# Optimization experiments

Measured on AMD Instinct MI355X. Metric: run time of the kernel, lower is better.

The kernel has to match this reference:

```python
import jax, jax.numpy as jnp
import numpy as np

B, L, D = 8, 4096, 256
G, K = 64, 8          # n_groups, group_size
N = G * K             # 512 slots
H = 8                 # attention heads
EPS = 1e-5

def _ln(x, g, b):
    m = jnp.mean(x, axis=-1, keepdims=True)
    v = jnp.var(x, axis=-1, keepdims=True)
    return (x - m) * jax.lax.rsqrt(v + EPS) * g + b

def _gelu(x):
    return jax.nn.gelu(x, approximate=False)  # torch nn.GELU default = exact erf

def setup_inputs() -> dict:
    key = jax.random.key(0)
    ks = jax.random.split(key, 24)
    s = 0.02
    d = {
        'X': jax.random.normal(ks[0], (B, L, D), jnp.float32),
        'S': jax.random.normal(ks[1], (B, N, D), jnp.float32),
        'Wg':  jax.random.normal(ks[2], (D, G)) * s,
        'Wk':  jax.random.normal(ks[3], (D, K)) * s,
        'Wm1': jax.random.normal(ks[4], (D, 2*D)) * s, 'bm1': jnp.zeros((2*D,)),
        'Wm2': jax.random.normal(ks[5], (2*D, D)) * s, 'bm2': jnp.zeros((D,)),
        'Wgt1': jax.random.normal(ks[6], (D, D)) * s, 'bgt1': jnp.zeros((D,)),
        'Wgt2': jax.random.normal(ks[7], (D, 1)) * s, 'bgt2': jnp.zeros((1,)),
        'Wqkv': jax.random.normal(ks[8], (D, 3*D)) * s, 'bqkv': jnp.zeros((3*D,)),
        'Wo':  jax.random.normal(ks[9], (D, D)) * s, 'bo': jnp.zeros((D,)),
        'aln_g': jnp.ones((D,)), 'aln_b': jnp.zeros((D,)),
        'Wu1': jax.random.normal(ks[10], (2*D, 2*D)) * s, 'bu1': jnp.zeros((2*D,)),
        'Wu2': jax.random.normal(ks[11], (2*D, D)) * s, 'bu2': jnp.zeros((D,)),
        'ln_g': jnp.ones((D,)), 'ln_b': jnp.zeros((D,)),
    }
    return d

def reference(X, S, Wg, Wk, Wm1, bm1, Wm2, bm2, Wgt1, bgt1, Wgt2, bgt2,
              Wqkv, bqkv, Wo, bo, aln_g, aln_b, Wu1, bu1, Wu2, bu2, ln_g, ln_b):
    # --- hierarchical routing (eval path: argmax one-hot) ---
    msg = _gelu(X @ Wm1 + bm1) @ Wm2 + bm2                 # (B,L,D)
    gate = jax.nn.sigmoid(_gelu(X @ Wgt1 + bgt1) @ Wgt2 + bgt2)  # (B,L,1)
    gm = msg * gate
    gidx = jnp.argmax(X @ Wg, axis=-1)                     # (B,L)
    kidx = jnp.argmax(X @ Wk, axis=-1)                     # (B,L)
    idx = gidx * K + kidx                                  # flat slot id in [0,N)
    full = jax.nn.one_hot(idx, N, dtype=X.dtype)           # (B,L,N)
    incoming = jnp.einsum('bln,bld->bnd', full, gm)        # (B,N,D)
    # --- slot self-attention ---
    qkv = S @ Wqkv + bqkv
    q, k, v = jnp.split(qkv, 3, axis=-1)
    dh = D // H
    q = q.reshape(B, N, H, dh); k = k.reshape(B, N, H, dh); v = v.reshape(B, N, H, dh)
    scores = jnp.einsum('bqhd,bkhd->bhqk', q, k) / jnp.sqrt(jnp.asarray(dh, X.dtype))
    attn = jax.nn.softmax(scores, axis=-1)
    o = jnp.einsum('bhqk,bkhd->bqhd', attn, v).reshape(B, N, D) @ Wo + bo
    S1 = _ln(S + o, aln_g, aln_b)
    # --- update ---
    cat = jnp.concatenate([S1, incoming], axis=-1)         # (B,N,2D)
    S2 = S1 + _gelu(cat @ Wu1 + bu1) @ Wu2 + bu2
    return _ln(S2, ln_g, ln_b)
```

## Files before the change

kernel.cpp:

```cpp
#include <hip/hip_runtime.h>

typedef __bf16 bf16_t;
typedef __bf16 bf16x8 __attribute__((ext_vector_type(8)));
typedef __bf16 bf16x4v __attribute__((ext_vector_type(4)));
typedef __bf16 bf16x2v __attribute__((ext_vector_type(2)));
typedef float f32x4 __attribute__((ext_vector_type(4)));
typedef unsigned long long u64;

#define LN_EPS 1e-5f

__device__ __forceinline__ float erf_fast(float a) {
  const float t = fabsf(a);
  const float s = a * a;
  float r;
  if (t > 0.921875f) {
    float u;
    r = fmaf(-1.72853470e-5f, t, 3.83197126e-4f);
    u = fmaf(-3.88396438e-3f, t, 2.42546219e-2f);
    r = fmaf(r, s, u);
    r = fmaf(r, t, 1.06777877e-1f);
    r = fmaf(r, t, -6.37245935e-1f);
    r = fmaf(r, t, -1.28717512e-1f);
    r = fmaf(r, t, t);
    r = 1.0f - __expf(-r);
    r = copysignf(r, a);
  } else {
    r = -5.96761703e-4f;
    r = fmaf(r, s, 4.99119423e-3f);
    r = fmaf(r, s, -2.67681349e-2f);
    r = fmaf(r, s, 1.12819925e-1f);
    r = fmaf(r, s, -3.76125336e-1f);
    r = fmaf(r, s, 1.28379166e-1f);
    r = fmaf(r, a, a);
  }
  return r;
}

__device__ __forceinline__ float gelu_f(float x) {
  const float h = 0.5f * x;
  return fmaf(h, erf_fast(x * 0.70710678118654752f), h);
}

__device__ __forceinline__ void async16(const bf16_t* g, bf16_t* l) {
  __builtin_amdgcn_global_load_lds(
      (const __attribute__((address_space(1))) void*)g,
      (__attribute__((address_space(3))) void*)l, 16, 0, 0);
}

__global__ __launch_bounds__(256)
void prep_kernel(const float* __restrict__ X, const float* __restrict__ S,
                 const float* __restrict__ Wg, const float* __restrict__ Wk,
                 const float* __restrict__ Wm1, const float* __restrict__ Wgt1,
                 const float* __restrict__ Wm2, const float* __restrict__ Wqkv,
                 const float* __restrict__ Wo, const float* __restrict__ Wu1,
                 const float* __restrict__ Wu2,
                 bf16_t* __restrict__ Xb, bf16_t* __restrict__ Sb,
                 bf16_t* __restrict__ W1t, bf16_t* __restrict__ W2t,
                 bf16_t* __restrict__ Wqkvt, bf16_t* __restrict__ Wot,
                 bf16_t* __restrict__ Wu1t, bf16_t* __restrict__ Wu2t,
                 float4* __restrict__ zbase)
{
  const int bid = blockIdx.x;
  const int t = threadIdx.x;
  if (bid < 8192) {
    const int i = bid * 256 + t;
    const float4 v = ((const float4*)X)[i];
    bf16x4v o; o[0]=(bf16_t)v.x; o[1]=(bf16_t)v.y; o[2]=(bf16_t)v.z; o[3]=(bf16_t)v.w;
    ((bf16x4v*)Xb)[i] = o;
  } else if (bid < 9216) {
    const int i = (bid - 8192) * 256 + t;
    const float4 v = ((const float4*)S)[i];
    bf16x4v o; o[0]=(bf16_t)v.x; o[1]=(bf16_t)v.y; o[2]=(bf16_t)v.z; o[3]=(bf16_t)v.w;
    ((bf16x4v*)Sb)[i] = o;
  } else if (bid < 10112) {
    const int n = bid - 9216;
    const int k = t;
    float v;
    if (n < 512)      v = Wm1[k * 512 + n];
    else if (n < 768) v = Wgt1[k * 256 + (n - 512)];
    else if (n < 832) v = Wg[k * 64 + (n - 768)];
    else if (n < 840) v = Wk[k * 8 + (n - 832)];
    else              v = 0.f;
    W1t[n * 256 + k] = (bf16_t)v;
  } else if (bid < 10368) {
    const int n = bid - 10112;
    for (int k = t; k < 512; k += 256) W2t[n * 512 + k] = (bf16_t)Wm2[k * 256 + n];
  } else if (bid < 11136) {
    const int n = bid - 10368;
    Wqkvt[n * 256 + t] = (bf16_t)Wqkv[t * 768 + n];
  } else if (bid < 11392) {
    const int n = bid - 11136;
    Wot[n * 256 + t] = (bf16_t)Wo[t * 256 + n];
  } else if (bid < 11904) {
    const int n = bid - 11392;
    for (int k = t; k < 512; k += 256) Wu1t[n * 512 + k] = (bf16_t)Wu1[k * 512 + n];
  } else if (bid < 12160) {
    const int n = bid - 11904;
    for (int k = t; k < 512; k += 256) Wu2t[n * 512 + k] = (bf16_t)Wu2[k * 256 + n];
  } else {
    zbase[(bid - 12160) * 256 + t] = make_float4(0.f, 0.f, 0.f, 0.f);
  }
}

__global__ __launch_bounds__(256, 2)
void g1_kernel(const bf16_t* __restrict__ A,
               const bf16_t* __restrict__ Bt,
               const float* __restrict__ bias, const float* __restrict__ bias2,
               bf16_t* __restrict__ h1,
               const float* __restrict__ wgt2, float* __restrict__ gatelin,
               u64* __restrict__ bitmap)
{
  const int m0 = blockIdx.x * 128;
  const int by = blockIdx.y;
  const int n0 = by * 128;
  const int t = threadIdx.x;
  const int w = t >> 6;
  const int lane = t & 63;
  const int wr = w >> 1, wc = w & 1;
  const int quad = lane >> 4, l15 = lane & 15;

  __shared__ bf16_t lA[128 * 32];
  __shared__ bf16_t lB[128 * 32];
  __shared__ float sWg[256];
  __shared__ int sKi[128];

  if (by >= 4 && by < 6) sWg[t] = wgt2[t];

  f32x4 acc[4][4];
#pragma unroll
  for (int mt = 0; mt < 4; ++mt)
#pragma unroll
    for (int nt = 0; nt < 4; ++nt)
      acc[mt][nt] = (f32x4){0.f, 0.f, 0.f, 0.f};

  const int srow = t >> 2;
  const int schunk = ((t & 3) ^ (srow & 3)) * 8;
  const int ko = ((quad ^ (l15 & 3)) << 3);

  for (int k0 = 0; k0 < 256; k0 += 32) {
#pragma unroll
    for (int i = 0; i < 2; ++i) {
      const int row = i * 64 + srow;
      async16(A + (size_t)(m0 + row) * 256 + k0 + schunk,
              lA + (size_t)(i * 256 + (t & 192)) * 8);
      async16(Bt + (size_t)(n0 + row) * 256 + k0 + schunk,
              lB + (size_t)(i * 256 + (t & 192)) * 8);
    }
    __syncthreads();
    bf16x8 af[4], bfr[4];
#pragma unroll
    for (int mt = 0; mt < 4; ++mt)
      af[mt] = *(const bf16x8*)&lA[(wr * 64 + mt * 16 + l15) * 32 + ko];
#pragma unroll
    for (int nt = 0; nt < 4; ++nt)
      bfr[nt] = *(const bf16x8*)&lB[(wc * 64 + nt * 16 + l15) * 32 + ko];
#pragma unroll
    for (int mt = 0; mt < 4; ++mt)
#pragma unroll
      for (int nt = 0; nt < 4; ++nt)
        acc[mt][nt] = __builtin_amdgcn_mfma_f32_16x16x32_bf16(bfr[nt], af[mt], acc[mt][nt], 0, 0, 0);
    __syncthreads();
  }

  if (by < 4) {
#pragma unroll
    for (int mt = 0; mt < 4; ++mt) {
      const int row = m0 + wr * 64 + mt * 16 + l15;
#pragma unroll
      for (int nt = 0; nt < 4; ++nt) {
        const int colb = n0 + wc * 64 + nt * 16 + quad * 4;
        const float4 bb = *(const float4*)&bias[colb];
        bf16x4v o;
        o[0] = (bf16_t)gelu_f(acc[mt][nt][0] + bb.x);
        o[1] = (bf16_t)gelu_f(acc[mt][nt][1] + bb.y);
        o[2] = (bf16_t)gelu_f(acc[mt][nt][2] + bb.z);
        o[3] = (bf16_t)gelu_f(acc[mt][nt][3] + bb.w);
        *(bf16x4v*)&h1[(size_t)row * 512 + colb] = o;
      }
    }
  } else if (by < 6) {
#pragma unroll
    for (int mt = 0; mt < 4; ++mt) {
      const int row = m0 + wr * 64 + mt * 16 + l15;
      float part = 0.f;
#pragma unroll
      for (int nt = 0; nt < 4; ++nt) {
        const int colb = n0 + wc * 64 + nt * 16 + quad * 4;
        const int c = colb - 512;
        const float4 bb = *(const float4*)&bias2[c];
        part = fmaf(gelu_f(acc[mt][nt][0] + bb.x), sWg[c + 0], part);
        part = fmaf(gelu_f(acc[mt][nt][1] + bb.y), sWg[c + 1], part);
        part = fmaf(gelu_f(acc[mt][nt][2] + bb.z), sWg[c + 2], part);
        part = fmaf(gelu_f(acc[mt][nt][3] + bb.w), sWg[c + 3], part);
      }
      part += __shfl_xor(part, 16, 64);
      part += __shfl_xor(part, 32, 64);
      if (lane < 16) atomicAdd(&gatelin[row], part);
    }
  } else {
    int bi[4];
#pragma unroll
    for (int mt = 0; mt < 4; ++mt) {
      if (wc == 0) {
        float mv = -1e30f; int mi = 0;
#pragma unroll
        for (int nt = 0; nt < 4; ++nt)
#pragma unroll
          for (int j = 0; j < 4; ++j) {
            const int gc = nt * 16 + quad * 4 + j;
            const float v = acc[mt][nt][j];
            if (v > mv || (v == mv && gc < mi)) { mv = v; mi = gc; }
          }
#pragma unroll
        for (int off = 16; off <= 32; off <<= 1) {
          const float ov = __shfl_xor(mv, off, 64);
          const int oi = __shfl_xor(mi, off, 64);
          if (ov > mv || (ov == mv && oi < mi)) { mv = ov; mi = oi; }
        }
        bi[mt] = mi;
      } else {
        float mv = -1e30f; int mi = 0;
        if (quad < 2) {
#pragma unroll
          for (int j = 0; j < 4; ++j) {
            const int kc = quad * 4 + j;
            const float v = acc[mt][0][j];
            if (v > mv || (v == mv && kc < mi)) { mv = v; mi = kc; }
          }
        }
#pragma unroll
        for (int off = 16; off <= 32; off <<= 1) {
          const float ov = __shfl_xor(mv, off, 64);
          const int oi = __shfl_xor(mi, off, 64);
          if (ov > mv || (ov == mv && oi < mi)) { mv = ov; mi = oi; }
        }
        if (lane < 16) sKi[wr * 64 + mt * 16 + l15] = mi;
      }
    }
    __syncthreads();
    if (wc == 0 && lane < 16) {
#pragma unroll
      for (int mt = 0; mt < 4; ++mt) {
        const int rl = wr * 64 + mt * 16 + l15;
        const int row = m0 + rl;
        const int idx = bi[mt] * 8 + sKi[rl];
        const int b = row >> 12, tok = row & 4095;
        atomicOr(&bitmap[(size_t)(b * 512 + idx) * 64 + (tok >> 6)],
                 1ull << (tok & 63));
      }
    }
  }
}

template<int MT, int EPI>
__global__ __launch_bounds__(256)
void gemm_kernel(const bf16_t* __restrict__ A, int lda,
                 const bf16_t* __restrict__ Bt, int K,
                 const float* __restrict__ bias, const float* __restrict__ bias2,
                 void* __restrict__ outp, int ldc,
                 const float* __restrict__ wgt2, float* __restrict__ gatelin,
                 u64* __restrict__ bitmap)
{
  constexpr int BM = MT * 32;
  constexpr int CA = BM * 4;
  const int m0 = blockIdx.x * BM;
  const int by = blockIdx.y;
  const int n0 = by * 128;
  const int t = threadIdx.x;
  const int w = t >> 6;
  const int lane = t & 63;
  const int wr = w >> 1, wc = w & 1;
  const int quad = lane >> 4, l15 = lane & 15;

  __shared__ bf16_t lA[BM * 32];
  __shared__ bf16_t lB[128 * 32];

  f32x4 acc[MT][4];
#pragma unroll
  for (int mt = 0; mt < MT; ++mt)
#pragma unroll
    for (int nt = 0; nt < 4; ++nt)
      acc[mt][nt] = (f32x4){0.f, 0.f, 0.f, 0.f};

  for (int k0 = 0; k0 < K; k0 += 32) {
    if constexpr (CA >= 256) {
#pragma unroll
      for (int i = 0; i < CA / 256; ++i) {
        const int c = i * 256 + t;
        async16(A + (size_t)(m0 + (c >> 2)) * lda + k0 + (c & 3) * 8,
                lA + (size_t)(i * 256 + (t & 192)) * 8);
      }
    } else {
      if (t < CA)
        async16(A + (size_t)(m0 + (t >> 2)) * lda + k0 + (t & 3) * 8,
                lA + (size_t)(t & 192) * 8);
    }
#pragma unroll
    for (int i = 0; i < 2; ++i) {
      const int c = i * 256 + t;
      async16(Bt + (size_t)(n0 + (c >> 2)) * K + k0 + (c & 3) * 8,
              lB + (size_t)(i * 256 + (t & 192)) * 8);
    }
    __syncthreads();
    bf16x8 af[MT], bfr[4];
    const int ko = quad * 8;
#pragma unroll
    for (int mt = 0; mt < MT; ++mt)
      af[mt] = *(const bf16x8*)&lA[(wr * MT * 16 + mt * 16 + l15) * 32 + ko];
#pragma unroll
    for (int nt = 0; nt < 4; ++nt)
      bfr[nt] = *(const bf16x8*)&lB[(wc * 64 + nt * 16 + l15) * 32 + ko];
#pragma unroll
    for (int mt = 0; mt < MT; ++mt)
#pragma unroll
      for (int nt = 0; nt < 4; ++nt)
        acc[mt][nt] = __builtin_amdgcn_mfma_f32_16x16x32_bf16(bfr[nt], af[mt], acc[mt][nt], 0, 0, 0);
    __syncthreads();
  }

#pragma unroll
  for (int mt = 0; mt < MT; ++mt) {
    const int row = m0 + wr * MT * 16 + mt * 16 + l15;
#pragma unroll
    for (int nt = 0; nt < 4; ++nt) {
      const int colb = n0 + wc * 64 + nt * 16 + quad * 4;
      const float4 bb = *(const float4*)&bias[colb];
      bf16x4v o;
      o[0]=(bf16_t)gelu_f(acc[mt][nt][0]+bb.x); o[1]=(bf16_t)gelu_f(acc[mt][nt][1]+bb.y);
      o[2]=(bf16_t)gelu_f(acc[mt][nt][2]+bb.z); o[3]=(bf16_t)gelu_f(acc[mt][nt][3]+bb.w);
      *(bf16x4v*)&((bf16_t*)outp)[(size_t)row * ldc + colb] = o;
    }
  }
  (void)bias2; (void)wgt2; (void)gatelin; (void)bitmap;
}

__global__ __launch_bounds__(256)
void pair64_kernel(const bf16_t* __restrict__ H, const bf16_t* __restrict__ W2t,
                   const float* __restrict__ bm2, const float* __restrict__ sumg,
                   float* __restrict__ incom,
                   const bf16_t* __restrict__ Sb, const bf16_t* __restrict__ Wqkvt,
                   const float* __restrict__ bqkv, bf16_t* __restrict__ qkvb,
                   bf16_t* __restrict__ Vt)
{
  int id = blockIdx.x;
  const bool first = id < 128;
  if (!first) id -= 128;
  const bf16_t* A  = first ? H : Sb;
  const bf16_t* Bt = first ? W2t : Wqkvt;
  const float* bias = first ? bm2 : bqkv;
  const int lda = first ? 512 : 256;
  const int K   = first ? 512 : 256;
  const int m0 = (id & 63) * 64;
  const int n0 = (id >> 6) * 128;
  const int t = threadIdx.x;
  const int w = t >> 6;
  const int lane = t & 63;
  const int wr = w >> 1, wc = w & 1;
  const int quad = lane >> 4, l15 = lane & 15;

  __shared__ bf16_t lA[64 * 32];
  __shared__ bf16_t lB[128 * 32];

  f32x4 acc[2][4];
#pragma unroll
  for (int mt = 0; mt < 2; ++mt)
#pragma unroll
    for (int nt = 0; nt < 4; ++nt)
      acc[mt][nt] = (f32x4){0.f, 0.f, 0.f, 0.f};

  for (int k0 = 0; k0 < K; k0 += 32) {
    async16(A + (size_t)(m0 + (t >> 2)) * lda + k0 + (t & 3) * 8,
            lA + (size_t)(t & 192) * 8);
#pragma unroll
    for (int i = 0; i < 2; ++i) {
      const int c = i * 256 + t;
      async16(Bt + (size_t)(n0 + (c >> 2)) * K + k0 + (c & 3) * 8,
              lB + (size_t)(i * 256 + (t & 192)) * 8);
    }
    __syncthreads();
    bf16x8 af[2], bfr[4];
    const int ko = quad * 8;
#pragma unroll
    for (int mt = 0; mt < 2; ++mt)
      af[mt] = *(const bf16x8*)&lA[(wr * 32 + mt * 16 + l15) * 32 + ko];
#pragma unroll
    for (int nt = 0; nt < 4; ++nt)
      bfr[nt] = *(const bf16x8*)&lB[(wc * 64 + nt * 16 + l15) * 32 + ko];
#pragma unroll
    for (int mt = 0; mt < 2; ++mt)
#pragma unroll
      for (int nt = 0; nt < 4; ++nt)
        acc[mt][nt] = __builtin_amdgcn_mfma_f32_16x16x32_bf16(bfr[nt], af[mt], acc[mt][nt], 0, 0, 0);
    __syncthreads();
  }

  if (first) {
#pragma unroll
    for (int mt = 0; mt < 2; ++mt) {
      const int row = m0 + wr * 32 + mt * 16 + l15;
      const float gt = sumg[row];
#pragma unroll
      for (int nt = 0; nt < 4; ++nt) {
        const int colb = n0 + wc * 64 + nt * 16 + quad * 4;
        const float4 bb = *(const float4*)&bias[colb];
        *(float4*)&incom[(size_t)row * 256 + colb] =
            make_float4(fmaf(gt, bb.x, acc[mt][nt][0]), fmaf(gt, bb.y, acc[mt][nt][1]),
                        fmaf(gt, bb.z, acc[mt][nt][2]), fmaf(gt, bb.w, acc[mt][nt][3]));
      }
    }
  } else if (n0 < 512) {
#pragma unroll
    for (int mt = 0; mt < 2; ++mt) {
      const int row = m0 + wr * 32 + mt * 16 + l15;
#pragma unroll
      for (int nt = 0; nt < 4; ++nt) {
        const int colb = n0 + wc * 64 + nt * 16 + quad * 4;
        const float4 bb = *(const float4*)&bias[colb];
        bf16x4v o; o[0]=(bf16_t)(acc[mt][nt][0]+bb.x); o[1]=(bf16_t)(acc[mt][nt][1]+bb.y);
        o[2]=(bf16_t)(acc[mt][nt][2]+bb.z); o[3]=(bf16_t)(acc[mt][nt][3]+bb.w);
        *(bf16x4v*)&qkvb[(size_t)row * 768 + colb] = o;
      }
    }
  } else {
#pragma unroll
    for (int mt = 0; mt < 2; ++mt) {
      const int row = m0 + wr * 32 + mt * 16 + l15;
      const int b = row >> 9, key = row & 511;
#pragma unroll
      for (int nt = 0; nt < 4; ++nt) {
        const int colb = n0 + wc * 64 + nt * 16 + quad * 4;
        const int c = colb - 512;
        const int h2 = c >> 5, dh = c & 31;
        const float4 bb = *(const float4*)&bias[colb];
        bf16_t* vb = Vt + ((size_t)(b * 8 + h2) * 32 + dh) * 512 + key;
        vb[0]   = (bf16_t)(acc[mt][nt][0] + bb.x);
        vb[512] = (bf16_t)(acc[mt][nt][1] + bb.y);
        vb[1024]= (bf16_t)(acc[mt][nt][2] + bb.z);
        vb[1536]= (bf16_t)(acc[mt][nt][3] + bb.w);
      }
    }
  }
}

__global__ __launch_bounds__(256)
void gather_kernel(const bf16_t* __restrict__ h1, const float* __restrict__ gatelin,
                   const float* __restrict__ bgt2, const u64* __restrict__ bitmap,
                   bf16_t* __restrict__ H, float* __restrict__ sumg)
{
  const int bs = blockIdx.x;
  const int b = bs >> 9;
  const int t = threadIdx.x;
  __shared__ u64 sw[64];
  if (t < 64) sw[t] = bitmap[(size_t)bs * 64 + t];
  __syncthreads();
  const float bg = bgt2[0];
  float a0 = 0.f, a1 = 0.f, sg = 0.f;
  for (int wd = 0; wd < 64; ++wd) {
    u64 word = sw[wd];
    while (word) {
      const int bit = __builtin_ctzll(word);
      word &= word - 1;
      const int l = (b << 12) + (wd << 6) + bit;
      const float g = 1.0f / (1.0f + __expf(-(gatelin[l] + bg)));
      const bf16x2v hv = *(const bf16x2v*)&h1[(size_t)l * 512 + t * 2];
      a0 = fmaf(g, (float)hv[0], a0);
      a1 = fmaf(g, (float)hv[1], a1);
      sg += g;
    }
  }
  bf16x2v o; o[0] = (bf16_t)a0; o[1] = (bf16_t)a1;
  *(bf16x2v*)&H[(size_t)bs * 512 + t * 2] = o;
  if (t == 0) sumg[bs] = sg;
}

__global__ __launch_bounds__(256)
void attn_kernel(const bf16_t* __restrict__ qkv, const bf16_t* __restrict__ Vt,
                 bf16_t* __restrict__ obuf)
{
  const int bid = blockIdx.x;
  const int qc = bid & 15;
  const int h = (bid >> 4) & 7;
  const int b = bid >> 7;
  const int t = threadIdx.x;
  const int w = t >> 6, lane = t & 63;
  const int quad = lane >> 4, l15 = lane & 15;

  __shared__ bf16_t sP[32 * 520];
  __shared__ float sL[32];

  bf16x8 qf[2];
#pragma unroll
  for (int mt = 0; mt < 2; ++mt) {
    const int row = b * 512 + qc * 32 + mt * 16 + l15;
    qf[mt] = *(const bf16x8*)&qkv[(size_t)row * 768 + h * 32 + quad * 8];
  }
  const float scale = 0.17677669529663687f;
  for (int kt = w; kt < 32; kt += 4) {
    const int key = b * 512 + kt * 16 + l15;
    const bf16x8 kf = *(const bf16x8*)&qkv[(size_t)key * 768 + 256 + h * 32 + quad * 8];
#pragma unroll
    for (int mt = 0; mt < 2; ++mt) {
      f32x4 c = (f32x4){0.f, 0.f, 0.f, 0.f};
      c = __builtin_amdgcn_mfma_f32_16x16x32_bf16(qf[mt], kf, c, 0, 0, 0);
#pragma unroll
      for (int r = 0; r < 4; ++r)
        sP[(mt * 16 + quad * 4 + r) * 520 + kt * 16 + l15] = (bf16_t)(c[r] * scale);
    }
  }
  __syncthreads();

#pragma unroll
  for (int ri = 0; ri < 8; ++ri) {
    const int row = w * 8 + ri;
    const bf16x8 sv = *(const bf16x8*)&sP[row * 520 + lane * 8];
    float sval[8];
    float mx = -1e30f;
#pragma unroll
    for (int j = 0; j < 8; ++j) { sval[j] = (float)sv[j]; mx = fmaxf(mx, sval[j]); }
#pragma unroll
    for (int off = 32; off; off >>= 1) mx = fmaxf(mx, __shfl_xor(mx, off, 64));
    float sum = 0.f;
    bf16x8 pv;
#pragma unroll
    for (int j = 0; j < 8; ++j) { const float e = __expf(sval[j] - mx); sum += e; pv[j] = (bf16_t)e; }
#pragma unroll
    for (int off = 32; off; off >>= 1) sum += __shfl_xor(sum, off, 64);
    *(bf16x8*)&sP[row * 520 + lane * 8] = pv;
    if (lane == 0) sL[row] = sum;
  }
  __syncthreads();

  const int wq = w >> 1, wd = w & 1;
  const bf16_t* vbase = Vt + ((size_t)(b * 8 + h) * 32 + wd * 16 + l15) * 512;
  const bf16_t* pbase = &sP[(wq * 16 + l15) * 520];
  f32x4 oacc = (f32x4){0.f, 0.f, 0.f, 0.f};
#pragma unroll
  for (int kt = 0; kt < 16; ++kt) {
    const bf16x8 af = *(const bf16x8*)&pbase[kt * 32 + quad * 8];
    const bf16x8 vf = *(const bf16x8*)&vbase[kt * 32 + quad * 8];
    oacc = __builtin_amdgcn_mfma_f32_16x16x32_bf16(vf, af, oacc, 0, 0, 0);
  }
  const int rowq = wq * 16 + l15;
  const float inv = 1.0f / sL[rowq];
  bf16x4v o;
#pragma unroll
  for (int r = 0; r < 4; ++r) o[r] = (bf16_t)(oacc[r] * inv);
  *(bf16x4v*)&obuf[(size_t)(b * 512 + qc * 32 + rowq) * 256 + h * 32 + wd * 16 + quad * 4] = o;
}

__global__ __launch_bounds__(256)
void wo_ln1_kernel(const bf16_t* __restrict__ obuf, const bf16_t* __restrict__ Wot,
                   const float* __restrict__ bo, const float* __restrict__ S,
                   const float* __restrict__ incom, const float* __restrict__ g,
                   const float* __restrict__ bb, float* __restrict__ S1f,
                   bf16_t* __restrict__ A4)
{
  const int m0 = blockIdx.x * 16;
  const int t = threadIdx.x;
  const int w = t >> 6, lane = t & 63;
  const int quad = lane >> 4, l15 = lane & 15;

  __shared__ bf16_t lA[16 * 32];
  __shared__ bf16_t lB[256 * 32];
  __shared__ float sSum[4][16];
  __shared__ float sSq[4][16];

  f32x4 acc[4];
#pragma unroll
  for (int nt = 0; nt < 4; ++nt) acc[nt] = (f32x4){0.f, 0.f, 0.f, 0.f};

  for (int k0 = 0; k0 < 256; k0 += 32) {
    if (t < 64)
      async16(obuf + (size_t)(m0 + (t >> 2)) * 256 + k0 + (t & 3) * 8, lA);
#pragma unroll
    for (int i = 0; i < 4; ++i) {
      const int c = i * 256 + t;
      async16(Wot + (size_t)(c >> 2) * 256 + k0 + (c & 3) * 8,
              lB + (size_t)(i * 256 + (t & 192)) * 8);
    }
    __syncthreads();
    const int ko = quad * 8;
    const bf16x8 af = *(const bf16x8*)&lA[l15 * 32 + ko];
#pragma unroll
    for (int nt = 0; nt < 4; ++nt) {
      const bf16x8 bfr = *(const bf16x8*)&lB[(w * 64 + nt * 16 + l15) * 32 + ko];
      acc[nt] = __builtin_amdgcn_mfma_f32_16x16x32_bf16(bfr, af, acc[nt], 0, 0, 0);
    }
    __syncthreads();
  }

  const int row = m0 + l15;
  float sum = 0.f, sq = 0.f;
#pragma unroll
  for (int nt = 0; nt < 4; ++nt) {
    const int colb = w * 64 + nt * 16 + quad * 4;
    const float4 bv = *(const float4*)&bo[colb];
    const float4 sv = *(const float4*)&S[(size_t)row * 256 + colb];
    float x0 = acc[nt][0] + bv.x + sv.x, x1 = acc[nt][1] + bv.y + sv.y;
    float x2 = acc[nt][2] + bv.z + sv.z, x3 = acc[nt][3] + bv.w + sv.w;
    acc[nt][0] = x0; acc[nt][1] = x1; acc[nt][2] = x2; acc[nt][3] = x3;
    sum += x0 + x1 + x2 + x3;
    sq += x0*x0 + x1*x1 + x2*x2 + x3*x3;
  }
  sum += __shfl_xor(sum, 16, 64); sum += __shfl_xor(sum, 32, 64);
  sq  += __shfl_xor(sq, 16, 64);  sq  += __shfl_xor(sq, 32, 64);
  if (lane < 16) { sSum[w][l15] = sum; sSq[w][l15] = sq; }
  __syncthreads();
  const float tot = sSum[0][l15] + sSum[1][l15] + sSum[2][l15] + sSum[3][l15];
  const float tq  = sSq[0][l15] + sSq[1][l15] + sSq[2][l15] + sSq[3][l15];
  const float mean = tot * 0.00390625f;
  const float var = tq * 0.00390625f - mean * mean;
  const float rstd = rsqrtf(var + LN_EPS);
#pragma unroll
  for (int nt = 0; nt < 4; ++nt) {
    const int colb = w * 64 + nt * 16 + quad * 4;
    const float4 gg = *(const float4*)&g[colb];
    const float4 bv = *(const float4*)&bb[colb];
    const float y0 = (acc[nt][0]-mean)*rstd*gg.x + bv.x;
    const float y1 = (acc[nt][1]-mean)*rstd*gg.y + bv.y;
    const float y2 = (acc[nt][2]-mean)*rstd*gg.z + bv.z;
    const float y3 = (acc[nt][3]-mean)*rstd*gg.w + bv.w;
    *(float4*)&S1f[(size_t)row * 256 + colb] = make_float4(y0, y1, y2, y3);
    bf16x4v yb; yb[0]=(bf16_t)y0; yb[1]=(bf16_t)y1; yb[2]=(bf16_t)y2; yb[3]=(bf16_t)y3;
    *(bf16x4v*)&A4[(size_t)row * 512 + colb] = yb;
    const float4 ic = *(const float4*)&incom[(size_t)row * 256 + colb];
    bf16x4v ib; ib[0]=(bf16_t)ic.x; ib[1]=(bf16_t)ic.y; ib[2]=(bf16_t)ic.z; ib[3]=(bf16_t)ic.w;
    *(bf16x4v*)&A4[(size_t)row * 512 + 256 + colb] = ib;
  }
}

__global__ __launch_bounds__(256)
void wu2_ln2_kernel(const bf16_t* __restrict__ U, const bf16_t* __restrict__ Wu2t,
                    const float* __restrict__ bu2, const float* __restrict__ S1f,
                    const float* __restrict__ g, const float* __restrict__ bb,
                    float* __restrict__ out)
{
  const int m0 = blockIdx.x * 16;
  const int t = threadIdx.x;
  const int w = t >> 6, lane = t & 63;
  const int quad = lane >> 4, l15 = lane & 15;

  __shared__ bf16_t lA[16 * 32];
  __shared__ bf16_t lB[256 * 32];
  __shared__ float sSum[4][16];
  __shared__ float sSq[4][16];

  f32x4 acc[4];
#pragma unroll
  for (int nt = 0; nt < 4; ++nt) acc[nt] = (f32x4){0.f, 0.f, 0.f, 0.f};

  for (int k0 = 0; k0 < 512; k0 += 32) {
    if (t < 64)
      async16(U + (size_t)(m0 + (t >> 2)) * 512 + k0 + (t & 3) * 8, lA);
#pragma unroll
    for (int i = 0; i < 4; ++i) {
      const int c = i * 256 + t;
      async16(Wu2t + (size_t)(c >> 2) * 512 + k0 + (c & 3) * 8,
              lB + (size_t)(i * 256 + (t & 192)) * 8);
    }
    __syncthreads();
    const int ko = quad * 8;
    const bf16x8 af = *(const bf16x8*)&lA[l15 * 32 + ko];
#pragma unroll
    for (int nt = 0; nt < 4; ++nt) {
      const bf16x8 bfr = *(const bf16x8*)&lB[(w * 64 + nt * 16 + l15) * 32 + ko];
      acc[nt] = __builtin_amdgcn_mfma_f32_16x16x32_bf16(bfr, af, acc[nt], 0, 0, 0);
    }
    __syncthreads();
  }

  const int row = m0 + l15;
  float sum = 0.f, sq = 0.f;
#pragma unroll
  for (int nt = 0; nt < 4; ++nt) {
    const int colb = w * 64 + nt * 16 + quad * 4;
    const float4 bv = *(const float4*)&bu2[colb];
    const float4 sv = *(const float4*)&S1f[(size_t)row * 256 + colb];
    float x0 = acc[nt][0] + bv.x + sv.x, x1 = acc[nt][1] + bv.y + sv.y;
    float x2 = acc[nt][2] + bv.z + sv.z, x3 = acc[nt][3] + bv.w + sv.w;
    acc[nt][0] = x0; acc[nt][1] = x1; acc[nt][2] = x2; acc[nt][3] = x3;
    sum += x0 + x1 + x2 + x3;
    sq += x0*x0 + x1*x1 + x2*x2 + x3*x3;
  }
  sum += __shfl_xor(sum, 16, 64); sum += __shfl_xor(sum, 32, 64);
  sq  += __shfl_xor(sq, 16, 64);  sq  += __shfl_xor(sq, 32, 64);
  if (lane < 16) { sSum[w][l15] = sum; sSq[w][l15] = sq; }
  __syncthreads();
  const float tot = sSum[0][l15] + sSum[1][l15] + sSum[2][l15] + sSum[3][l15];
  const float tq  = sSq[0][l15] + sSq[1][l15] + sSq[2][l15] + sSq[3][l15];
  const float mean = tot * 0.00390625f;
  const float var = tq * 0.00390625f - mean * mean;
  const float rstd = rsqrtf(var + LN_EPS);
#pragma unroll
  for (int nt = 0; nt < 4; ++nt) {
    const int colb = w * 64 + nt * 16 + quad * 4;
    const float4 gg = *(const float4*)&g[colb];
    const float4 bv = *(const float4*)&bb[colb];
    *(float4*)&out[(size_t)row * 256 + colb] = make_float4(
        (acc[nt][0]-mean)*rstd*gg.x + bv.x, (acc[nt][1]-mean)*rstd*gg.y + bv.y,
        (acc[nt][2]-mean)*rstd*gg.z + bv.z, (acc[nt][3]-mean)*rstd*gg.w + bv.w);
  }
}

extern "C" void kernel_launch(void* const* d_in, const int* in_sizes, int n_in,
                              void* d_out, int out_size, void* d_ws, size_t ws_size,
                              hipStream_t stream)
{
  (void)in_sizes; (void)n_in; (void)out_size; (void)ws_size;
  const float* X    = (const float*)d_in[0];
  const float* S    = (const float*)d_in[1];
  const float* Wg   = (const float*)d_in[2];
  const float* Wk   = (const float*)d_in[3];
  const float* Wm1  = (const float*)d_in[4];
  const float* bm1  = (const float*)d_in[5];
  const float* Wm2  = (const float*)d_in[6];
  const float* bm2  = (const float*)d_in[7];
  const float* Wgt1 = (const float*)d_in[8];
  const float* bgt1 = (const float*)d_in[9];
  const float* Wgt2 = (const float*)d_in[10];
  const float* bgt2 = (const float*)d_in[11];
  const float* Wqkv = (const float*)d_in[12];
  const float* bqkv = (const float*)d_in[13];
  const float* Wo   = (const float*)d_in[14];
  const float* bo   = (const float*)d_in[15];
  const float* alng = (const float*)d_in[16];
  const float* alnb = (const float*)d_in[17];
  const float* Wu1  = (const float*)d_in[18];
  const float* bu1  = (const float*)d_in[19];
  const float* Wu2  = (const float*)d_in[20];
  const float* bu2  = (const float*)d_in[21];
  const float* lng  = (const float*)d_in[22];
  const float* lnb  = (const float*)d_in[23];

  char* p = (char*)d_ws;
  auto carve = [&](size_t bytes) { char* r = p; p += bytes; return r; };
  bf16_t* Xb    = (bf16_t*)carve(16777216);
  bf16_t* Sb    = (bf16_t*)carve(2097152);
  bf16_t* W1t   = (bf16_t*)carve(458752);
  bf16_t* W2t   = (bf16_t*)carve(262144);
  bf16_t* Wqkvt = (bf16_t*)carve(393216);
  bf16_t* Wot   = (bf16_t*)carve(131072);
  bf16_t* Wu1t  = (bf16_t*)carve(524288);
  bf16_t* Wu2t  = (bf16_t*)carve(262144);
  bf16_t* h1    = (bf16_t*)carve(33554432);
  u64*    bitmap  = (u64*)carve(2097152);
  float*  gatelin = (float*)carve(131072);
  float*  incom = (float*)carve(4194304);
  bf16_t* qkvb  = (bf16_t*)carve(6291456);
  bf16_t* Vt    = (bf16_t*)carve(2097152);
  bf16_t* obuf  = (bf16_t*)carve(2097152);
  float*  S1f   = (float*)carve(4194304);
  bf16_t* A4    = (bf16_t*)carve(4194304);
  bf16_t* U     = (bf16_t*)carve(4194304);
  float*  sumg  = (float*)carve(16384);
  bf16_t* H = U;

  prep_kernel<<<12704, 256, 0, stream>>>(X, S, Wg, Wk, Wm1, Wgt1, Wm2, Wqkv, Wo, Wu1, Wu2,
                                         Xb, Sb, W1t, W2t, Wqkvt, Wot, Wu1t, Wu2t,
                                         (float4*)bitmap);
  g1_kernel<<<dim3(256, 7), 256, 0, stream>>>(Xb, W1t, bm1, bgt1, h1,
                                              Wgt2, gatelin, bitmap);
  gather_kernel<<<4096, 256, 0, stream>>>(h1, gatelin, bgt2, bitmap, H, sumg);
  pair64_kernel<<<512, 256, 0, stream>>>(H, W2t, bm2, sumg, incom,
                                         Sb, Wqkvt, bqkv, qkvb, Vt);
  attn_kernel<<<1024, 256, 0, stream>>>(qkvb, Vt, obuf);
  wo_ln1_kernel<<<256, 256, 0, stream>>>(obuf, Wot, bo, S, incom, alng, alnb, S1f, A4);
  gemm_kernel<2,5><<<dim3(64,4), 256, 0, stream>>>(A4, 512, Wu1t, 512, bu1, nullptr, U, 512,
                                                   nullptr, nullptr, nullptr);
  wu2_ln2_kernel<<<256, 256, 0, stream>>>(U, Wu2t, bu2, S1f, lng, lnb, (float*)d_out);
}
```

Baseline: 255.9 us.

## Regroup QKV GEMM into g1 launch and msg GEMM into attention launch

Moves the slot QKV projection blocks into the big g1 GEMM launch as extra blocks, and moves the message Wm2 GEMM blocks into the attention launch. This removes one kernel launch and lets independent work fill idle CUs during tail phases. In exchange, the g1 kernel now carries the extra branch code and shared-memory layout for both paths, which may affect occupancy. Mixing block types with different runtimes can also create load imbalance.

After: 249.1 us. 2.7% less time.

```diff
diff --git a/kernel.cpp b/kernel.cpp
--- a/kernel.cpp
+++ b/kernel.cpp
@@ -103,16 +103,17 @@
 }
 
 __global__ __launch_bounds__(256, 2)
-void g1_kernel(const bf16_t* __restrict__ A,
-               const bf16_t* __restrict__ Bt,
-               const float* __restrict__ bias, const float* __restrict__ bias2,
-               bf16_t* __restrict__ h1,
-               const float* __restrict__ wgt2, float* __restrict__ gatelin,
-               u64* __restrict__ bitmap)
+void g1qkv_kernel(const bf16_t* __restrict__ A,
+                  const bf16_t* __restrict__ Bt,
+                  const float* __restrict__ bias, const float* __restrict__ bias2,
+                  bf16_t* __restrict__ h1,
+                  const float* __restrict__ wgt2, float* __restrict__ gatelin,
+                  u64* __restrict__ bitmap,
+                  const bf16_t* __restrict__ Sb, const bf16_t* __restrict__ Wqkvt,
+                  const float* __restrict__ bqkv, bf16_t* __restrict__ qkvb,
+                  bf16_t* __restrict__ Vt)
 {
-  const int m0 = blockIdx.x * 128;
-  const int by = blockIdx.y;
-  const int n0 = by * 128;
+  const int bid = blockIdx.x;
   const int t = threadIdx.x;
   const int w = t >> 6;
   const int lane = t & 63;
@@ -123,6 +124,83 @@
   __shared__ bf16_t lB[128 * 32];
   __shared__ float sWg[256];
   __shared__ int sKi[128];
+
+  if (bid >= 1792) {
+    const int id = bid - 1792;
+    const int m0 = (id & 63) * 64;
+    const int n0 = (id >> 6) * 128;
+
+    f32x4 acc[2][4];
+#pragma unroll
+    for (int mt = 0; mt < 2; ++mt)
+#pragma unroll
+      for (int nt = 0; nt < 4; ++nt)
+        acc[mt][nt] = (f32x4){0.f, 0.f, 0.f, 0.f};
+
+    for (int k0 = 0; k0 < 256; k0 += 32) {
+      async16(Sb + (size_t)(m0 + (t >> 2)) * 256 + k0 + (t & 3) * 8,
+              lA + (size_t)(t & 192) * 8);
+#pragma unroll
+      for (int i = 0; i < 2; ++i) {
+        const int c = i * 256 + t;
+        async16(Wqkvt + (size_t)(n0 + (c >> 2)) * 256 + k0 + (c & 3) * 8,
+                lB + (size_t)(i * 256 + (t & 192)) * 8);
+      }
+      __syncthreads();
+      bf16x8 af[2], bfr[4];
+      const int ko = quad * 8;
+#pragma unroll
+      for (int mt = 0; mt < 2; ++mt)
+        af[mt] = *(const bf16x8*)&lA[(wr * 32 + mt * 16 + l15) * 32 + ko];
+#pragma unroll
+      for (int nt = 0; nt < 4; ++nt)
+        bfr[nt] = *(const bf16x8*)&lB[(wc * 64 + nt * 16 + l15) * 32 + ko];
+#pragma unroll
+      for (int mt = 0; mt < 2; ++mt)
+#pragma unroll
+        for (int nt = 0; nt < 4; ++nt)
+          acc[mt][nt] = __builtin_amdgcn_mfma_f32_16x16x32_bf16(bfr[nt], af[mt], acc[mt][nt], 0, 0, 0);
+      __syncthreads();
+    }
+
+    if (n0 < 512) {
+#pragma unroll
+      for (int mt = 0; mt < 2; ++mt) {
+        const int row = m0 + wr * 32 + mt * 16 + l15;
+#pragma unroll
+        for (int nt = 0; nt < 4; ++nt) {
+          const int colb = n0 + wc * 64 + nt * 16 + quad * 4;
+          const float4 bb = *(const float4*)&bqkv[colb];
+          bf16x4v o; o[0]=(bf16_t)(acc[mt][nt][0]+bb.x); o[1]=(bf16_t)(acc[mt][nt][1]+bb.y);
+          o[2]=(bf16_t)(acc[mt][nt][2]+bb.z); o[3]=(bf16_t)(acc[mt][nt][3]+bb.w);
+          *(bf16x4v*)&qkvb[(size_t)row * 768 + colb] = o;
+        }
+      }
+    } else {
+#pragma unroll
+      for (int mt = 0; mt < 2; ++mt) {
+        const int row = m0 + wr * 32 + mt * 16 + l15;
+        const int b = row >> 9, key = row & 511;
+#pragma unroll
+        for (int nt = 0; nt < 4; ++nt) {
+          const int colb = n0 + wc * 64 + nt * 16 + quad * 4;
+          const int c = colb - 512;
+          const int h2 = c >> 5, dh = c & 31;
+          const float4 bb = *(const float4*)&bqkv[colb];
+          bf16_t* vb = Vt + ((size_t)(b * 8 + h2) * 32 + dh) * 512 + key;
+          vb[0]   = (bf16_t)(acc[mt][nt][0] + bb.x);
+          vb[512] = (bf16_t)(acc[mt][nt][1] + bb.y);
+          vb[1024]= (bf16_t)(acc[mt][nt][2] + bb.z);
+          vb[1536]= (bf16_t)(acc[mt][nt][3] + bb.w);
+        }
+      }
+    }
+    return;
+  }
+
+  const int m0 = (bid & 255) * 128;
+  const int by = bid >> 8;
+  const int n0 = by * 128;
 
   if (by >= 4 && by < 6) sWg[t] = wgt2[t];
 
@@ -332,114 +410,6 @@
     }
   }
   (void)bias2; (void)wgt2; (void)gatelin; (void)bitmap;
-}
-
-__global__ __launch_bounds__(256)
-void pair64_kernel(const bf16_t* __restrict__ H, const bf16_t* __restrict__ W2t,
-                   const float* __restrict__ bm2, const float* __restrict__ sumg,
-                   float* __restrict__ incom,
-                   const bf16_t* __restrict__ Sb, const bf16_t* __restrict__ Wqkvt,
-                   const float* __restrict__ bqkv, bf16_t* __restrict__ qkvb,
-                   bf16_t* __restrict__ Vt)
-{
-  int id = blockIdx.x;
-  const bool first = id < 128;
-  if (!first) id -= 128;
-  const bf16_t* A  = first ? H : Sb;
-  const bf16_t* Bt = first ? W2t : Wqkvt;
-  const float* bias = first ? bm2 : bqkv;
-  const int lda = first ? 512 : 256;
-  const int K   = first ? 512 : 256;
-  const int m0 = (id & 63) * 64;
-  const int n0 = (id >> 6) * 128;
-  const int t = threadIdx.x;
-  const int w = t >> 6;
-  const int lane = t & 63;
-  const int wr = w >> 1, wc = w & 1;
-  const int quad = lane >> 4, l15 = lane & 15;
-
-  __shared__ bf16_t lA[64 * 32];
-  __shared__ bf16_t lB[128 * 32];
-
-  f32x4 acc[2][4];
-#pragma unroll
-  for (int mt = 0; mt < 2; ++mt)
-#pragma unroll
-    for (int nt = 0; nt < 4; ++nt)
-      acc[mt][nt] = (f32x4){0.f, 0.f, 0.f, 0.f};
-
-  for (int k0 = 0; k0 < K; k0 += 32) {
-    async16(A + (size_t)(m0 + (t >> 2)) * lda + k0 + (t & 3) * 8,
-            lA + (size_t)(t & 192) * 8);
-#pragma unroll
-    for (int i = 0; i < 2; ++i) {
-      const int c = i * 256 + t;
-      async16(Bt + (size_t)(n0 + (c >> 2)) * K + k0 + (c & 3) * 8,
-              lB + (size_t)(i * 256 + (t & 192)) * 8);
-    }
-    __syncthreads();
-    bf16x8 af[2], bfr[4];
-    const int ko = quad * 8;
-#pragma unroll
-    for (int mt = 0; mt < 2; ++mt)
-      af[mt] = *(const bf16x8*)&lA[(wr * 32 + mt * 16 + l15) * 32 + ko];
-#pragma unroll
-    for (int nt = 0; nt < 4; ++nt)
-      bfr[nt] = *(const bf16x8*)&lB[(wc * 64 + nt * 16 + l15) * 32 + ko];
-#pragma unroll
-    for (int mt = 0; mt < 2; ++mt)
-#pragma unroll
-      for (int nt = 0; nt < 4; ++nt)
-        acc[mt][nt] = __builtin_amdgcn_mfma_f32_16x16x32_bf16(bfr[nt], af[mt], acc[mt][nt], 0, 0, 0);
-    __syncthreads();
-  }
-
-  if (first) {
-#pragma unroll
-    for (int mt = 0; mt < 2; ++mt) {
-      const int row = m0 + wr * 32 + mt * 16 + l15;
-      const float gt = sumg[row];
-#pragma unroll
-      for (int nt = 0; nt < 4; ++nt) {
-        const int colb = n0 + wc * 64 + nt * 16 + quad * 4;
-        const float4 bb = *(const float4*)&bias[colb];
-        *(float4*)&incom[(size_t)row * 256 + colb] =
-            make_float4(fmaf(gt, bb.x, acc[mt][nt][0]), fmaf(gt, bb.y, acc[mt][nt][1]),
-                        fmaf(gt, bb.z, acc[mt][nt][2]), fmaf(gt, bb.w, acc[mt][nt][3]));
-      }
-    }
-  } else if (n0 < 512) {
-#pragma unroll
-    for (int mt = 0; mt < 2; ++mt) {
-      const int row = m0 + wr * 32 + mt * 16 + l15;
-#pragma unroll
-      for (int nt = 0; nt < 4; ++nt) {
-        const int colb = n0 + wc * 64 + nt * 16 + quad * 4;
-        const float4 bb = *(const float4*)&bias[colb];
-        bf16x4v o; o[0]=(bf16_t)(acc[mt][nt][0]+bb.x); o[1]=(bf16_t)(acc[mt][nt][1]+bb.y);
-        o[2]=(bf16_t)(acc[mt][nt][2]+bb.z); o[3]=(bf16_t)(acc[mt][nt][3]+bb.w);
-        *(bf16x4v*)&qkvb[(size_t)row * 768 + colb] = o;
-      }
-    }
-  } else {
-#pragma unroll
-    for (int mt = 0; mt < 2; ++mt) {
-      const int row = m0 + wr * 32 + mt * 16 + l15;
-      const int b = row >> 9, key = row & 511;
-#pragma unroll
-      for (int nt = 0; nt < 4; ++nt) {
-        const int colb = n0 + wc * 64 + nt * 16 + quad * 4;
-        const int c = colb - 512;
-        const int h2 = c >> 5, dh = c & 31;
-        const float4 bb = *(const float4*)&bias[colb];
-        bf16_t* vb = Vt + ((size_t)(b * 8 + h2) * 32 + dh) * 512 + key;
-        vb[0]   = (bf16_t)(acc[mt][nt][0] + bb.x);
-        vb[512] = (bf16_t)(acc[mt][nt][1] + bb.y);
-        vb[1024]= (bf16_t)(acc[mt][nt][2] + bb.z);
-        vb[1536]= (bf16_t)(acc[mt][nt][3] + bb.w);
-      }
-    }
-  }
 }
 
 __global__ __launch_bounds__(256)
@@ -474,19 +444,80 @@
 }
 
 __global__ __launch_bounds__(256)
-void attn_kernel(const bf16_t* __restrict__ qkv, const bf16_t* __restrict__ Vt,
-                 bf16_t* __restrict__ obuf)
+void g2attn_kernel(const bf16_t* __restrict__ qkv, const bf16_t* __restrict__ Vt,
+                   bf16_t* __restrict__ obuf,
+                   const bf16_t* __restrict__ H, const bf16_t* __restrict__ W2t,
+                   const float* __restrict__ bm2, const float* __restrict__ sumg,
+                   float* __restrict__ incom)
 {
   const int bid = blockIdx.x;
-  const int qc = bid & 15;
-  const int h = (bid >> 4) & 7;
-  const int b = bid >> 7;
   const int t = threadIdx.x;
   const int w = t >> 6, lane = t & 63;
   const int quad = lane >> 4, l15 = lane & 15;
 
   __shared__ bf16_t sP[32 * 520];
   __shared__ float sL[32];
+
+  if (bid < 128) {
+    const int wr = w >> 1, wc = w & 1;
+    const int m0 = (bid & 63) * 64;
+    const int n0 = (bid >> 6) * 128;
+    bf16_t* lA = sP;
+    bf16_t* lB = sP + 64 * 32;
+
+    f32x4 acc[2][4];
+#pragma unroll
+    for (int mt = 0; mt < 2; ++mt)
+#pragma unroll
+      for (int nt = 0; nt < 4; ++nt)
+        acc[mt][nt] = (f32x4){0.f, 0.f, 0.f, 0.f};
+
+    for (int k0 = 0; k0 < 512; k0 += 32) {
+      async16(H + (size_t)(m0 + (t >> 2)) * 512 + k0 + (t & 3) * 8,
+              lA + (size_t)(t & 192) * 8);
+#pragma unroll
+      for (int i = 0; i < 2; ++i) {
+        const int c = i * 256 + t;
+        async16(W2t + (size_t)(n0 + (c >> 2)) * 512 + k0 + (c & 3) * 8,
+                lB + (size_t)(i * 256 + (t & 192)) * 8);
+      }
+      __syncthreads();
+      bf16x8 af[2], bfr[4];
+      const int ko = quad * 8;
+#pragma unroll
+      for (int mt = 0; mt < 2; ++mt)
+        af[mt] = *(const bf16x8*)&lA[(wr * 32 + mt * 16 + l15) * 32 + ko];
+#pragma unroll
+      for (int nt = 0; nt < 4; ++nt)
+        bfr[nt] = *(const bf16x8*)&lB[(wc * 64 + nt * 16 + l15) * 32 + ko];
+#pragma unroll
+      for (int mt = 0; mt < 2; ++mt)
+#pragma unroll
+        for (int nt = 0; nt < 4; ++nt)
+          acc[mt][nt] = __builtin_amdgcn_mfma_f32_16x16x32_bf16(bfr[nt], af[mt], acc[mt][nt], 0, 0, 0);
+      __syncthreads();
+    }
+
+#pragma unroll
+    for (int mt = 0; mt < 2; ++mt) {
+      const int row = m0 + wr * 32 + mt * 16 + l15;
+      const float gt = sumg[row];
+#pragma unroll
+      for (int nt = 0; nt < 4; ++nt) {
+        const int colb = n0 + wc * 64 + nt * 16 + quad * 4;
+        const float4 bb = *(const float4*)&bm2[colb];
+        *(float4*)&incom[(size_t)row * 256 + colb] =
+            make_float4(fmaf(gt, bb.x, acc[mt][nt][0]), fmaf(gt, bb.y, acc[mt][nt][1]),
+                        fmaf(gt, bb.z, acc[mt][nt][2]), fmaf(gt, bb.w, acc[mt][nt][3]));
+      }
+    }
+    return;
+  }
+
+  const int abid = bid - 128;
+  const int qc = abid & 15;
+  const int h = (abid >> 4) & 7;
+  const int b = abid >> 7;
 
   bf16x8 qf[2];
 #pragma unroll
@@ -758,12 +789,12 @@
   prep_kernel<<<12704, 256, 0, stream>>>(X, S, Wg, Wk, Wm1, Wgt1, Wm2, Wqkv, Wo, Wu1, Wu2,
                                          Xb, Sb, W1t, W2t, Wqkvt, Wot, Wu1t, Wu2t,
                                          (float4*)bitmap);
-  g1_kernel<<<dim3(256, 7), 256, 0, stream>>>(Xb, W1t, bm1, bgt1, h1,
-                                              Wgt2, gatelin, bitmap);
+  g1qkv_kernel<<<2176, 256, 0, stream>>>(Xb, W1t, bm1, bgt1, h1,
+                                         Wgt2, gatelin, bitmap,
+                                         Sb, Wqkvt, bqkv, qkvb, Vt);
   gather_kernel<<<4096, 256, 0, stream>>>(h1, gatelin, bgt2, bitmap, H, sumg);
-  pair64_kernel<<<512, 256, 0, stream>>>(H, W2t, bm2, sumg, incom,
-                                         Sb, Wqkvt, bqkv, qkvb, Vt);
-  attn_kernel<<<1024, 256, 0, stream>>>(qkvb, Vt, obuf);
+  g2attn_kernel<<<1152, 256, 0, stream>>>(qkvb, Vt, obuf,
+                                          H, W2t, bm2, sumg, incom);
   wo_ln1_kernel<<<256, 256, 0, stream>>>(obuf, Wot, bo, S, incom, alng, alnb, S1f, A4);
   gemm_kernel<2,5><<<dim3(64,4), 256, 0, stream>>>(A4, 512, Wu1t, 512, bu1, nullptr, U, 512,
                                                    nullptr, nullptr, nullptr);
```
